# Kernel tuning notes

Measured on AMD Instinct MI355X. Metric: run time of the kernel, lower is better.

The kernel has to match this reference:

```python
import jax, jax.numpy as jnp
import numpy as np
from jax.scipy.linalg import expm

N_WIRES = 9
N_LAYERS = 4
EMBED = 512
BATCH = 64
D = 2 ** N_WIRES
P = N_WIRES * N_LAYERS * 2  # gate angles per sample


def _apply_gate(st, g, w):
    # st: (D, 2,...,2) complex64; apply 2x2 gate g on wire w
    st = jnp.moveaxis(st, 1 + w, -1)
    st = st @ g.T  # new[a] = sum_b g[a,b] old[b]
    return jnp.moveaxis(st, -1, 1 + w)


def _apply_cnot(st, c, t):
    st = jnp.moveaxis(st, (1 + c, 1 + t), (-2, -1))
    st = jnp.concatenate([st[..., 0:1, :], st[..., 1:2, ::-1]], axis=-2)
    return jnp.moveaxis(st, (-2, -1), (1 + c, 1 + t))


def _build_unitary(params):
    # simulate circuit on all D basis states at once (identity input)
    st = jnp.eye(D, dtype=jnp.complex64).reshape((D,) + (2,) * N_WIRES)
    idx = 0
    for _ in range(N_LAYERS):
        for w in range(N_WIRES):
            thy = params[idx]
            thz = params[idx + 1]
            idx += 2
            c = jnp.cos(thy * 0.5).astype(jnp.complex64)
            s = jnp.sin(thy * 0.5).astype(jnp.complex64)
            ry = jnp.stack([jnp.stack([c, -s]), jnp.stack([s, c])])
            ep = jnp.exp(0.5j * thz.astype(jnp.complex64))  # exp(i*thz/2)
            zero = jnp.zeros((), jnp.complex64)
            rz = jnp.stack([jnp.stack([jnp.conj(ep), zero]), jnp.stack([zero, ep])])
            st = _apply_gate(st, rz @ ry, w)  # Ry then Rz, fused
        for w in range(N_WIRES - 1):
            st = _apply_cnot(st, w, w + 1)
        st = _apply_cnot(st, N_WIRES - 1, 0)  # ring entangler (n_wires>1)
    # row index = input basis state i -> column i of U; take real part
    return jnp.real(st.reshape(D, D)).T


def _forward(t, w1, b1, w2, b2):
    h = jax.nn.silu(t[:, None] @ w1 + b1)          # (B, EMBED)
    params = h @ w2 + b2                            # (B, P)
    p_sg = jax.lax.stop_gradient(params)            # torch uses .detach() for the circuit
    U_stack = jax.vmap(_build_unitary)(p_sg)        # (B, D, D)
    B = t.shape[0]
    A = jnp.zeros((B, D * D), params.dtype).at[:, :P].set(params).reshape(B, D, D)
    A_skew = (A - jnp.swapaxes(A, -1, -2)) * 0.01
    U_diff = jax.vmap(expm)(A_skew)                 # (B, D, D)
    return jnp.einsum('bij,bjk->bik', U_stack, U_diff)


def setup_inputs() -> dict:
    key = jax.random.key(0)
    k_t, k1, kb1, k2, kb2 = jax.random.split(key, 5)
    t = jax.random.normal(k_t, (BATCH,), jnp.float32)
    w1 = jax.random.normal(k1, (1, EMBED), jnp.float32)
    b1 = jax.random.normal(kb1, (EMBED,), jnp.float32) * 0.1
    w2 = jax.random.normal(k2, (EMBED, P), jnp.float32) / np.sqrt(EMBED)
    b2 = jax.random.normal(kb2, (P,), jnp.float32) * 0.1
    return {"t": t, "w1": w1, "b1": b1, "w2": w2, "b2": b2}


def reference(t, w1, b1, w2, b2):
    return _forward(t, w1, b1, w2, b2)
```

## Files before the change

kernel.cpp:

```cpp
#include <hip/hip_runtime.h>
#include <math.h>


__device__ __forceinline__ float2 cmul(float2 a, float2 b){
  return make_float2(fmaf(a.x, b.x, -a.y*b.y), fmaf(a.x, b.y, a.y*b.x));
}

__device__ __forceinline__ float2 pk_fma_lo(float2 a, float2 b, float2 c){
  float2 d;
  asm("v_pk_fma_f32 %0, %1, %2, %3 op_sel:[0,0,0] op_sel_hi:[0,1,1]"
      : "=v"(d) : "v"(a), "v"(b), "v"(c));
  return d;
}
__device__ __forceinline__ float2 pk_fma_hi(float2 a, float2 b, float2 c){
  float2 d;
  asm("v_pk_fma_f32 %0, %1, %2, %3 op_sel:[1,0,0] op_sel_hi:[1,1,1]"
      : "=v"(d) : "v"(a), "v"(b), "v"(c));
  return d;
}
__device__ __forceinline__ float2 pk_mul_hi(float2 a, float2 b){
  float2 d;
  asm("v_pk_mul_f32 %0, %1, %2 op_sel:[1,0] op_sel_hi:[1,1]"
      : "=v"(d) : "v"(a), "v"(b));
  return d;
}

__device__ __forceinline__ int Fperm(int x){
  int S = x ^ (x >> 1); S ^= S >> 2; S ^= S >> 4; S ^= S >> 8;
  return (S & 0xFF) | ((((x >> 8) ^ S) & 1) << 8);
}
__device__ __forceinline__ int physmap(int x){ return x ^ ((x >> 4) & 15); }

template<int STRIDE>
__device__ __forceinline__ void apply_gate_pk(float2 amp[8], const float4* gq){
  const float4 a0 = gq[0], a1 = gq[1], a2 = gq[2], a3 = gq[3];
  const float2 P00 = make_float2(a0.x,a0.y), Q00 = make_float2(a0.z,a0.w);
  const float2 P01 = make_float2(a1.x,a1.y), Q01 = make_float2(a1.z,a1.w);
  const float2 P10 = make_float2(a2.x,a2.y), Q10 = make_float2(a2.z,a2.w);
  const float2 P11 = make_float2(a3.x,a3.y), Q11 = make_float2(a3.z,a3.w);
  #pragma unroll
  for (int b = 0; b < 8; ++b){
    if (b & STRIDE) continue;
    const float2 u = amp[b], v = amp[b + STRIDE];
    amp[b]          = pk_fma_lo(u,P00, pk_fma_hi(u,Q00, pk_fma_lo(v,P01, pk_mul_hi(v,Q01))));
    amp[b + STRIDE] = pk_fma_lo(u,P10, pk_fma_hi(u,Q10, pk_fma_lo(v,P11, pk_mul_hi(v,Q11))));
  }
}

__global__ __launch_bounds__(576)
void prep_kernel(const float* __restrict__ t,  const float* __restrict__ w1,
                 const float* __restrict__ b1, const float* __restrict__ w2,
                 const float* __restrict__ b2, float* __restrict__ prep){
  __shared__ float sh[512];
  __shared__ float part[8][72];
  __shared__ float spar[72];
  const int s = blockIdx.x;
  const float ts = t[s];
  for (int k = threadIdx.x; k < 512; k += 576){
    const float z = fmaf(ts, w1[k], b1[k]);
    sh[k] = z / (1.f + expf(-z));
  }
  __syncthreads();
  {
    const int p = threadIdx.x % 72, c = threadIdx.x / 72;
    float acc = 0.f;
    const int k0 = c*64;
    for (int k = k0; k < k0 + 64; ++k) acc = fmaf(sh[k], w2[k*72 + p], acc);
    part[c][p] = acc;
  }
  __syncthreads();
  if (threadIdx.x < 72){
    const int p = threadIdx.x;
    float acc = b2[p];
    #pragma unroll
    for (int c = 0; c < 8; ++c) acc += part[c][p];
    spar[p] = acc;
  }
  __syncthreads();
  float* pb = prep + s*768;
  if (threadIdx.x < 36){
    const int g = threadIdx.x;
    const float thy = spar[2*g], thz = spar[2*g + 1];
    float sy, cy, zi, zr;
    sincosf(0.5f*thy, &sy, &cy);
    sincosf(0.5f*thz, &zi, &zr);
    float4* gq = (float4*)(pb + g*16);
    gq[0] = make_float4( zr*cy, -zi*cy,  zi*cy,  zr*cy);
    gq[1] = make_float4(-zr*sy,  zi*sy, -zi*sy, -zr*sy);
    gq[2] = make_float4( zr*sy,  zi*sy, -zi*sy,  zr*sy);
    gq[3] = make_float4( zr*cy,  zi*cy, -zi*cy,  zr*cy);
  }
  if (threadIdx.x >= 64 && threadIdx.x < 136){
    const int j = threadIdx.x - 64;
    pb[576 + j] = (j == 0) ? 0.f : 0.01f*spar[j];
  }
  if (threadIdx.x == 0){
    float th2 = 0.f;
    for (int j = 1; j < 72; ++j){ const float v = 0.01f*spar[j]; th2 = fmaf(v, v, th2); }
    const float th = sqrtf(th2);
    float alpha, beta;
    if (th > 1e-6f){
      alpha = sinf(th)/th;
      const float s2 = sinf(0.5f*th);
      beta = 2.f*s2*s2/th2;
    } else { alpha = 1.f - th2/6.f; beta = 0.5f; }
    pb[648] = cosf(th);
    pb[649] = alpha;
    pb[650] = beta;
  }
}

__global__ __launch_bounds__(512, 6)
void sim_kernel(const float* __restrict__ prep, float* __restrict__ out){
  __shared__ __align__(16) float2 st[8][512];
  const int s    = blockIdx.x & 63;
  const int cb   = blockIdx.x >> 6;
  const int wid  = threadIdx.x >> 6;
  const int lane = threadIdx.x & 63;
  const int col  = cb*8 + wid;
  const float* gp = prep + s*768;
  float2* const S = st[wid];

  float2 amp[8];
  {
    float2 base = make_float2(1.f, 0.f);
    #pragma unroll
    for (int w = 0; w < 6; ++w){
      const int xb = (lane >> (5 - w)) & 1;
      const int ib = (col  >> (8 - w)) & 1;
      const float2 ge = *(const float2*)(gp + 16*w + (xb*2 + ib)*4);
      base = cmul(base, ge);
    }
    const int i6 = (col >> 2) & 1, i7 = (col >> 1) & 1, i8 = col & 1;
    float2 G6[2], G7[2], G8[2];
    #pragma unroll
    for (int r = 0; r < 2; ++r){
      G6[r] = *(const float2*)(gp + 16*6 + (r*2 + i6)*4);
      G7[r] = *(const float2*)(gp + 16*7 + (r*2 + i7)*4);
      G8[r] = *(const float2*)(gp + 16*8 + (r*2 + i8)*4);
    }
    #pragma unroll
    for (int j = 0; j < 8; ++j){
      const float2 tj = cmul(cmul(G6[(j>>2)&1], G7[(j>>1)&1]), G8[j&1]);
      amp[j] = cmul(base, tj);
    }
    const int bFI = physmap(Fperm(lane << 3));
    #pragma unroll
    for (int j = 0; j < 8; ++j) S[bFI ^ physmap(Fperm(j))] = amp[j];
  }

  const int base1 = (lane << 3) ^ ((lane >> 1) & 15);
  const int hq = lane >> 3, lq = lane & 7;
  const int base2 = (hq << 6) ^ ((hq << 2) & 15) ^ lq;
  const int base3 = lane ^ (lane >> 4);
  const int baseF = physmap(Fperm(lane));

  #pragma unroll
  for (int L = 1; L < 4; ++L){
    const float* gl = gp + L*9*16;
    #pragma unroll
    for (int j = 0; j < 8; ++j) amp[j] = S[base1 ^ j];
    apply_gate_pk<4>(amp, (const float4*)(gl + 6*16));
    apply_gate_pk<2>(amp, (const float4*)(gl + 7*16));
    apply_gate_pk<1>(amp, (const float4*)(gl + 8*16));
    #pragma unroll
    for (int j = 0; j < 8; ++j) S[base1 ^ j] = amp[j];
    #pragma unroll
    for (int j = 0; j < 8; ++j) amp[j] = S[base2 ^ ((j << 3) ^ (j >> 1))];
    apply_gate_pk<4>(amp, (const float4*)(gl + 3*16));
    apply_gate_pk<2>(amp, (const float4*)(gl + 4*16));
    apply_gate_pk<1>(amp, (const float4*)(gl + 5*16));
    #pragma unroll
    for (int j = 0; j < 8; ++j) S[base2 ^ ((j << 3) ^ (j >> 1))] = amp[j];
    #pragma unroll
    for (int j = 0; j < 8; ++j) amp[j] = S[base3 ^ ((j << 6) ^ ((4*j) & 15))];
    apply_gate_pk<4>(amp, (const float4*)(gl + 0*16));
    apply_gate_pk<2>(amp, (const float4*)(gl + 1*16));
    apply_gate_pk<1>(amp, (const float4*)(gl + 2*16));
    #pragma unroll
    for (int j = 0; j < 8; ++j) S[baseF ^ physmap(Fperm(j << 6))] = amp[j];
  }

  __syncthreads();
  #pragma unroll
  for (int rep = 0; rep < 2; ++rep){
    const int a  = (threadIdx.x >> 1) + rep*256;
    const int q  = threadIdx.x & 1;
    const int pa = a ^ ((a >> 4) & 15);
    float4 vv;
    vv.x = st[q*4 + 0][pa].x;
    vv.y = st[q*4 + 1][pa].x;
    vv.z = st[q*4 + 2][pa].x;
    vv.w = st[q*4 + 3][pa].x;
    *(float4*)&out[(size_t)s*262144 + (size_t)a*512 + cb*8 + q*4] = vv;
  }
}

__global__ __launch_bounds__(288)
void corr_kernel(const float* __restrict__ prep, float* __restrict__ out){
  __shared__ float part[16][18];
  __shared__ float srow[16][2];
  const int s  = blockIdx.x >> 5;
  const int rg = blockIdx.x & 31;
  const float* pp = prep + s*768;
  const int lr = threadIdx.x / 18;
  const int q  = threadIdx.x - lr*18;
  float* rowp = out + (size_t)s*262144 + (size_t)(rg*16 + lr)*512;
  const float4 x  = *(const float4*)(rowp + q*4);
  const float4 vv = *(const float4*)(pp + 576 + q*4);
  part[lr][q] = fmaf(x.x,vv.x, fmaf(x.y,vv.y, fmaf(x.z,vv.z, x.w*vv.w)));
  __syncthreads();
  if (threadIdx.x < 16){
    const int row = threadIdx.x;
    float uv = 0.f;
    #pragma unroll
    for (int k = 0; k < 18; ++k) uv += part[row][k];
    const float u0 = out[(size_t)s*262144 + (size_t)(rg*16 + row)*512];
    const float cth = pp[648], alpha = pp[649], beta = pp[650];
    srow[row][0] = fmaf(alpha, u0, -beta*uv);
    srow[row][1] = cth*u0 - alpha*uv;
  }
  __syncthreads();
  const float w = srow[lr][0];
  float4 o;
  o.x = fmaf(w, vv.x, x.x); o.y = fmaf(w, vv.y, x.y);
  o.z = fmaf(w, vv.z, x.z); o.w = fmaf(w, vv.w, x.w);
  if (q == 0) o.x = srow[lr][1];
  *(float4*)(rowp + q*4) = o;
}

extern "C" void kernel_launch(void* const* d_in, const int* in_sizes, int n_in,
                              void* d_out, int out_size, void* d_ws, size_t ws_size,
                              hipStream_t stream){
  const float* t  = (const float*)d_in[0];
  const float* w1 = (const float*)d_in[1];
  const float* b1 = (const float*)d_in[2];
  const float* w2 = (const float*)d_in[3];
  const float* b2 = (const float*)d_in[4];
  float* out  = (float*)d_out;
  float* prep = (float*)d_ws;
  prep_kernel<<<64,   576, 0, stream>>>(t, w1, b1, w2, b2, prep);
  sim_kernel <<<4096, 512, 0, stream>>>(prep, out);
  corr_kernel<<<2048, 288, 0, stream>>>(prep, out);
}
```

Measured before the change: 172.8 us.

## Split gates into real Ry rotations plus deferred diagonal Rz phase

Each fused complex Rz·Ry gate in layers 1-3 becomes a real Ry rotation, applied with scalar-operand packed FMAs (two ops per output instead of four). The Rz phases for a layer are commuted through the rotations and applied as one diagonal multiply per amplitude, built from a per-lane factor and a per-register factor that prep_kernel precomputes. The prep layout and offsets change to match, and the occupancy hint is raised from 6 to 8 waves. This trades complex FMA work for a per-layer phase multiply and extra loads of prep data.

Result: faster. 148.7 us (-13.9%).

```diff
diff --git a/kernel.cpp b/kernel.cpp
--- a/kernel.cpp
+++ b/kernel.cpp
@@ -6,22 +6,46 @@
   return make_float2(fmaf(a.x, b.x, -a.y*b.y), fmaf(a.x, b.y, a.y*b.x));
 }
 
-__device__ __forceinline__ float2 pk_fma_lo(float2 a, float2 b, float2 c){
+__device__ __forceinline__ float2 pk_fma_s_lo(float2 s2, float2 b, float2 c){
+  float2 d;
+  asm("v_pk_fma_f32 %0, %1, %2, %3 op_sel:[0,0,0] op_sel_hi:[0,1,1]"
+      : "=v"(d) : "s"(s2), "v"(b), "v"(c));
+  return d;
+}
+__device__ __forceinline__ float2 pk_mul_s_hi(float2 s2, float2 b){
+  float2 d;
+  asm("v_pk_mul_f32 %0, %1, %2 op_sel:[1,0] op_sel_hi:[1,1]"
+      : "=v"(d) : "s"(s2), "v"(b));
+  return d;
+}
+__device__ __forceinline__ float2 pk_fma_vs_lo(float2 a, float2 b, float2 c){
+  float2 d;
+  asm("v_pk_fma_f32 %0, %1, %2, %3 op_sel:[0,0,0] op_sel_hi:[0,1,1]"
+      : "=v"(d) : "v"(a), "s"(b), "v"(c));
+  return d;
+}
+__device__ __forceinline__ float2 pk_mul_vs_hi(float2 a, float2 b){
+  float2 d;
+  asm("v_pk_mul_f32 %0, %1, %2 op_sel:[1,0] op_sel_hi:[1,1]"
+      : "=v"(d) : "v"(a), "s"(b));
+  return d;
+}
+__device__ __forceinline__ float2 pk_fma_vv_lo(float2 a, float2 b, float2 c){
   float2 d;
   asm("v_pk_fma_f32 %0, %1, %2, %3 op_sel:[0,0,0] op_sel_hi:[0,1,1]"
       : "=v"(d) : "v"(a), "v"(b), "v"(c));
   return d;
 }
-__device__ __forceinline__ float2 pk_fma_hi(float2 a, float2 b, float2 c){
-  float2 d;
-  asm("v_pk_fma_f32 %0, %1, %2, %3 op_sel:[1,0,0] op_sel_hi:[1,1,1]"
-      : "=v"(d) : "v"(a), "v"(b), "v"(c));
-  return d;
-}
-__device__ __forceinline__ float2 pk_mul_hi(float2 a, float2 b){
+__device__ __forceinline__ float2 pk_mul_vv_hi(float2 a, float2 b){
   float2 d;
   asm("v_pk_mul_f32 %0, %1, %2 op_sel:[1,0] op_sel_hi:[1,1]"
       : "=v"(d) : "v"(a), "v"(b));
+  return d;
+}
+__device__ __forceinline__ float2 pk_swapneg(float2 c, float2 n){
+  float2 d;
+  asm("v_pk_mul_f32 %0, %1, %2 op_sel:[1,0] op_sel_hi:[0,1]"
+      : "=v"(d) : "v"(c), "v"(n));
   return d;
 }
 
@@ -32,18 +56,15 @@
 __device__ __forceinline__ int physmap(int x){ return x ^ ((x >> 4) & 15); }
 
 template<int STRIDE>
-__device__ __forceinline__ void apply_gate_pk(float2 amp[8], const float4* gq){
-  const float4 a0 = gq[0], a1 = gq[1], a2 = gq[2], a3 = gq[3];
-  const float2 P00 = make_float2(a0.x,a0.y), Q00 = make_float2(a0.z,a0.w);
-  const float2 P01 = make_float2(a1.x,a1.y), Q01 = make_float2(a1.z,a1.w);
-  const float2 P10 = make_float2(a2.x,a2.y), Q10 = make_float2(a2.z,a2.w);
-  const float2 P11 = make_float2(a3.x,a3.y), Q11 = make_float2(a3.z,a3.w);
+__device__ __forceinline__ void apply_rot(float2 amp[8], const float2* rp){
+  const float2 R0 = rp[0];
+  const float2 R1 = rp[1];
   #pragma unroll
   for (int b = 0; b < 8; ++b){
     if (b & STRIDE) continue;
     const float2 u = amp[b], v = amp[b + STRIDE];
-    amp[b]          = pk_fma_lo(u,P00, pk_fma_hi(u,Q00, pk_fma_lo(v,P01, pk_mul_hi(v,Q01))));
-    amp[b + STRIDE] = pk_fma_lo(u,P10, pk_fma_hi(u,Q10, pk_fma_lo(v,P11, pk_mul_hi(v,Q11))));
+    amp[b]          = pk_fma_s_lo(R0, u, pk_mul_s_hi(R0, v));
+    amp[b + STRIDE] = pk_fma_s_lo(R1, u, pk_mul_s_hi(R1, v));
   }
 }
 
@@ -77,24 +98,53 @@
     spar[p] = acc;
   }
   __syncthreads();
-  float* pb = prep + s*768;
-  if (threadIdx.x < 36){
-    const int g = threadIdx.x;
-    const float thy = spar[2*g], thz = spar[2*g + 1];
+  float* pb = prep + s*1024;
+  const int tid = threadIdx.x;
+  if (tid < 192){
+    const int l = tid >> 6, m = tid & 63;
+    float2 acc = make_float2(1.f, 0.f);
+    #pragma unroll
+    for (int w = 3; w < 9; ++w){
+      const float thz = spar[2*(9*(l+1) + w) + 1];
+      float zi, zr; sincosf(0.5f*thz, &zi, &zr);
+      const int bit = (m >> (8 - w)) & 1;
+      acc = cmul(acc, make_float2(zr, bit ? zi : -zi));
+    }
+    pb[128 + l*256 + 128 + m*2]     = acc.x;
+    pb[128 + l*256 + 128 + m*2 + 1] = acc.y;
+  } else if (tid < 216){
+    const int q = tid - 192, l = q >> 3, j = q & 7;
+    float2 acc = make_float2(1.f, 0.f);
+    #pragma unroll
+    for (int w = 0; w < 3; ++w){
+      const float thz = spar[2*(9*(l+1) + w) + 1];
+      float zi, zr; sincosf(0.5f*thz, &zi, &zr);
+      const int bit = (j >> (2 - w)) & 1;
+      acc = cmul(acc, make_float2(zr, bit ? zi : -zi));
+    }
+    float* o = pb + 128 + l*256 + 64 + j*4;
+    o[0] = acc.x; o[1] = acc.y; o[2] = -acc.y; o[3] = acc.x;
+  } else if (tid < 243){
+    const int q = tid - 216, l = q / 9, w = q - l*9;
+    const float thy = spar[2*(9*(l+1) + w)];
+    float sy, cy; sincosf(0.5f*thy, &sy, &cy);
+    float* o = pb + 128 + l*256 + w*4;
+    o[0] = cy; o[1] = -sy; o[2] = sy; o[3] = cy;
+  } else if (tid < 252){
+    const int w = tid - 243;
+    const float thy = spar[2*w], thz = spar[2*w + 1];
     float sy, cy, zi, zr;
     sincosf(0.5f*thy, &sy, &cy);
     sincosf(0.5f*thz, &zi, &zr);
-    float4* gq = (float4*)(pb + g*16);
-    gq[0] = make_float4( zr*cy, -zi*cy,  zi*cy,  zr*cy);
-    gq[1] = make_float4(-zr*sy,  zi*sy, -zi*sy, -zr*sy);
-    gq[2] = make_float4( zr*sy,  zi*sy, -zi*sy,  zr*sy);
-    gq[3] = make_float4( zr*cy,  zi*cy, -zi*cy,  zr*cy);
-  }
-  if (threadIdx.x >= 64 && threadIdx.x < 136){
-    const int j = threadIdx.x - 64;
-    pb[576 + j] = (j == 0) ? 0.f : 0.01f*spar[j];
-  }
-  if (threadIdx.x == 0){
+    float* o = pb + w*8;
+    o[0] =  zr*cy; o[1] = -zi*cy;
+    o[2] = -zr*sy; o[3] =  zi*sy;
+    o[4] =  zr*sy; o[5] =  zi*sy;
+    o[6] =  zr*cy; o[7] =  zi*cy;
+  } else if (tid < 324){
+    const int j = tid - 252;
+    pb[896 + j] = (j == 0) ? 0.f : 0.01f*spar[j];
+  } else if (tid == 324){
     float th2 = 0.f;
     for (int j = 1; j < 72; ++j){ const float v = 0.01f*spar[j]; th2 = fmaf(v, v, th2); }
     const float th = sqrtf(th2);
@@ -104,13 +154,13 @@
       const float s2 = sinf(0.5f*th);
       beta = 2.f*s2*s2/th2;
     } else { alpha = 1.f - th2/6.f; beta = 0.5f; }
-    pb[648] = cosf(th);
-    pb[649] = alpha;
-    pb[650] = beta;
-  }
-}
-
-__global__ __launch_bounds__(512, 6)
+    pb[968] = cosf(th);
+    pb[969] = alpha;
+    pb[970] = beta;
+  }
+}
+
+__global__ __launch_bounds__(512, 8)
 void sim_kernel(const float* __restrict__ prep, float* __restrict__ out){
   __shared__ __align__(16) float2 st[8][512];
   const int s    = blockIdx.x & 63;
@@ -118,8 +168,9 @@
   const int wid  = threadIdx.x >> 6;
   const int lane = threadIdx.x & 63;
   const int col  = cb*8 + wid;
-  const float* gp = prep + s*768;
+  const float* gp = prep + s*1024;
   float2* const S = st[wid];
+  const float2 NEG1P1 = make_float2(-1.f, 1.f);
 
   float2 amp[8];
   {
@@ -128,16 +179,16 @@
     for (int w = 0; w < 6; ++w){
       const int xb = (lane >> (5 - w)) & 1;
       const int ib = (col  >> (8 - w)) & 1;
-      const float2 ge = *(const float2*)(gp + 16*w + (xb*2 + ib)*4);
+      const float2 ge = *(const float2*)(gp + 8*w + (xb*2 + ib)*2);
       base = cmul(base, ge);
     }
     const int i6 = (col >> 2) & 1, i7 = (col >> 1) & 1, i8 = col & 1;
     float2 G6[2], G7[2], G8[2];
     #pragma unroll
     for (int r = 0; r < 2; ++r){
-      G6[r] = *(const float2*)(gp + 16*6 + (r*2 + i6)*4);
-      G7[r] = *(const float2*)(gp + 16*7 + (r*2 + i7)*4);
-      G8[r] = *(const float2*)(gp + 16*8 + (r*2 + i8)*4);
+      G6[r] = *(const float2*)(gp + 8*6 + (r*2 + i6)*2);
+      G7[r] = *(const float2*)(gp + 8*7 + (r*2 + i7)*2);
+      G8[r] = *(const float2*)(gp + 8*8 + (r*2 + i8)*2);
     }
     #pragma unroll
     for (int j = 0; j < 8; ++j){
@@ -156,27 +207,38 @@
   const int baseF = physmap(Fperm(lane));
 
   #pragma unroll
-  for (int L = 1; L < 4; ++L){
-    const float* gl = gp + L*9*16;
+  for (int L = 0; L < 3; ++L){
+    const float* lb = gp + 128 + L*256;
     #pragma unroll
     for (int j = 0; j < 8; ++j) amp[j] = S[base1 ^ j];
-    apply_gate_pk<4>(amp, (const float4*)(gl + 6*16));
-    apply_gate_pk<2>(amp, (const float4*)(gl + 7*16));
-    apply_gate_pk<1>(amp, (const float4*)(gl + 8*16));
+    apply_rot<4>(amp, (const float2*)(lb + 6*4));
+    apply_rot<2>(amp, (const float2*)(lb + 7*4));
+    apply_rot<1>(amp, (const float2*)(lb + 8*4));
     #pragma unroll
     for (int j = 0; j < 8; ++j) S[base1 ^ j] = amp[j];
     #pragma unroll
     for (int j = 0; j < 8; ++j) amp[j] = S[base2 ^ ((j << 3) ^ (j >> 1))];
-    apply_gate_pk<4>(amp, (const float4*)(gl + 3*16));
-    apply_gate_pk<2>(amp, (const float4*)(gl + 4*16));
-    apply_gate_pk<1>(amp, (const float4*)(gl + 5*16));
+    apply_rot<4>(amp, (const float2*)(lb + 3*4));
+    apply_rot<2>(amp, (const float2*)(lb + 4*4));
+    apply_rot<1>(amp, (const float2*)(lb + 5*4));
     #pragma unroll
     for (int j = 0; j < 8; ++j) S[base2 ^ ((j << 3) ^ (j >> 1))] = amp[j];
     #pragma unroll
     for (int j = 0; j < 8; ++j) amp[j] = S[base3 ^ ((j << 6) ^ ((4*j) & 15))];
-    apply_gate_pk<4>(amp, (const float4*)(gl + 0*16));
-    apply_gate_pk<2>(amp, (const float4*)(gl + 1*16));
-    apply_gate_pk<1>(amp, (const float4*)(gl + 2*16));
+    apply_rot<4>(amp, (const float2*)(lb + 0*4));
+    apply_rot<2>(amp, (const float2*)(lb + 1*4));
+    apply_rot<1>(amp, (const float2*)(lb + 2*4));
+    {
+      const float2 A = *(const float2*)(lb + 128 + lane*2);
+      #pragma unroll
+      for (int j = 0; j < 8; ++j){
+        const float2 P = *(const float2*)(lb + 64 + j*4);
+        const float2 Q = *(const float2*)(lb + 64 + j*4 + 2);
+        const float2 C = pk_fma_vs_lo(A, P, pk_mul_vs_hi(A, Q));
+        const float2 Dn = pk_swapneg(C, NEG1P1);
+        amp[j] = pk_fma_vv_lo(amp[j], C, pk_mul_vv_hi(amp[j], Dn));
+      }
+    }
     #pragma unroll
     for (int j = 0; j < 8; ++j) S[baseF ^ physmap(Fperm(j << 6))] = amp[j];
   }
@@ -202,12 +264,12 @@
   __shared__ float srow[16][2];
   const int s  = blockIdx.x >> 5;
   const int rg = blockIdx.x & 31;
-  const float* pp = prep + s*768;
+  const float* pp = prep + s*1024;
   const int lr = threadIdx.x / 18;
   const int q  = threadIdx.x - lr*18;
   float* rowp = out + (size_t)s*262144 + (size_t)(rg*16 + lr)*512;
   const float4 x  = *(const float4*)(rowp + q*4);
-  const float4 vv = *(const float4*)(pp + 576 + q*4);
+  const float4 vv = *(const float4*)(pp + 896 + q*4);
   part[lr][q] = fmaf(x.x,vv.x, fmaf(x.y,vv.y, fmaf(x.z,vv.z, x.w*vv.w)));
   __syncthreads();
   if (threadIdx.x < 16){
@@ -216,7 +278,7 @@
     #pragma unroll
     for (int k = 0; k < 18; ++k) uv += part[row][k];
     const float u0 = out[(size_t)s*262144 + (size_t)(rg*16 + row)*512];
-    const float cth = pp[648], alpha = pp[649], beta = pp[650];
+    const float cth = pp[968], alpha = pp[969], beta = pp[970];
     srow[row][0] = fmaf(alpha, u0, -beta*uv);
     srow[row][1] = cth*u0 - alpha*uv;
   }
```

## Fuse parameter prep into sim kernel and factor Rz gates into diagonal phases

Applied to the files above, without the earlier changes.

Drops the separate prep kernel. Each sim block now recomputes the MLP, sin/cos and gate tables into LDS, which removes one launch and the global round-trip. Layers 2-4 split each gate into a real Ry rotation followed by one combined diagonal phase built from precomputed per-index angle tables, so the per-gate complex multiplies shrink. The corr kernel is restructured into fewer, larger blocks that reduce with wavefront shuffles instead of LDS. In exchange, every one of the 4096 blocks redoes a 512x72 matvec, which adds redundant compute and w2 reads.

Result: slower. 187.9 us (+8.8%).

```diff
diff --git a/kernel.cpp b/kernel.cpp
--- a/kernel.cpp
+++ b/kernel.cpp
@@ -5,25 +5,24 @@
 __device__ __forceinline__ float2 cmul(float2 a, float2 b){
   return make_float2(fmaf(a.x, b.x, -a.y*b.y), fmaf(a.x, b.y, a.y*b.x));
 }
-
 __device__ __forceinline__ float2 pk_fma_lo(float2 a, float2 b, float2 c){
   float2 d;
   asm("v_pk_fma_f32 %0, %1, %2, %3 op_sel:[0,0,0] op_sel_hi:[0,1,1]"
       : "=v"(d) : "v"(a), "v"(b), "v"(c));
   return d;
 }
-__device__ __forceinline__ float2 pk_fma_hi(float2 a, float2 b, float2 c){
-  float2 d;
-  asm("v_pk_fma_f32 %0, %1, %2, %3 op_sel:[1,0,0] op_sel_hi:[1,1,1]"
-      : "=v"(d) : "v"(a), "v"(b), "v"(c));
-  return d;
-}
 __device__ __forceinline__ float2 pk_mul_hi(float2 a, float2 b){
   float2 d;
   asm("v_pk_mul_f32 %0, %1, %2 op_sel:[1,0] op_sel_hi:[1,1]"
       : "=v"(d) : "v"(a), "v"(b));
   return d;
 }
+__device__ __forceinline__ float2 pk_swapneg(float2 c, float2 n){
+  float2 d;
+  asm("v_pk_mul_f32 %0, %1, %2 op_sel:[1,0] op_sel_hi:[0,1]"
+      : "=v"(d) : "v"(c), "v"(n));
+  return d;
+}
 
 __device__ __forceinline__ int Fperm(int x){
   int S = x ^ (x >> 1); S ^= S >> 2; S ^= S >> 4; S ^= S >> 8;
@@ -32,69 +31,104 @@
 __device__ __forceinline__ int physmap(int x){ return x ^ ((x >> 4) & 15); }
 
 template<int STRIDE>
-__device__ __forceinline__ void apply_gate_pk(float2 amp[8], const float4* gq){
-  const float4 a0 = gq[0], a1 = gq[1], a2 = gq[2], a3 = gq[3];
-  const float2 P00 = make_float2(a0.x,a0.y), Q00 = make_float2(a0.z,a0.w);
-  const float2 P01 = make_float2(a1.x,a1.y), Q01 = make_float2(a1.z,a1.w);
-  const float2 P10 = make_float2(a2.x,a2.y), Q10 = make_float2(a2.z,a2.w);
-  const float2 P11 = make_float2(a3.x,a3.y), Q11 = make_float2(a3.z,a3.w);
+__device__ __forceinline__ void apply_rot(float2 amp[8], float4 rc){
+  const float2 R0 = make_float2(rc.x, rc.y);
+  const float2 R1 = make_float2(rc.z, rc.w);
   #pragma unroll
   for (int b = 0; b < 8; ++b){
     if (b & STRIDE) continue;
     const float2 u = amp[b], v = amp[b + STRIDE];
-    amp[b]          = pk_fma_lo(u,P00, pk_fma_hi(u,Q00, pk_fma_lo(v,P01, pk_mul_hi(v,Q01))));
-    amp[b + STRIDE] = pk_fma_lo(u,P10, pk_fma_hi(u,Q10, pk_fma_lo(v,P11, pk_mul_hi(v,Q11))));
-  }
-}
-
-__global__ __launch_bounds__(576)
-void prep_kernel(const float* __restrict__ t,  const float* __restrict__ w1,
-                 const float* __restrict__ b1, const float* __restrict__ w2,
-                 const float* __restrict__ b2, float* __restrict__ prep){
-  __shared__ float sh[512];
-  __shared__ float part[8][72];
+    amp[b]          = pk_fma_lo(R0, u, pk_mul_hi(R0, v));
+    amp[b + STRIDE] = pk_fma_lo(R1, u, pk_mul_hi(R1, v));
+  }
+}
+
+#define LDS_L1G 0
+#define LDS_ROT 72
+#define LDS_BPH 180
+#define LDS_APH 288
+#define BUF_FLOATS 1160
+
+__global__ __launch_bounds__(512, 6)
+void sim_kernel(const float* __restrict__ t,  const float* __restrict__ w1,
+                const float* __restrict__ b1, const float* __restrict__ w2,
+                const float* __restrict__ b2,
+                float* __restrict__ out, float* __restrict__ ws){
+  __shared__ __align__(16) float2 st[8][512];
+  __shared__ __align__(16) float buf[BUF_FLOATS];
   __shared__ float spar[72];
-  const int s = blockIdx.x;
-  const float ts = t[s];
-  for (int k = threadIdx.x; k < 512; k += 576){
-    const float z = fmaf(ts, w1[k], b1[k]);
-    sh[k] = z / (1.f + expf(-z));
-  }
-  __syncthreads();
+  const int s    = blockIdx.x & 63;
+  const int cb   = blockIdx.x >> 6;
+  const int tid  = threadIdx.x;
+  const int wid  = tid >> 6;
+  const int lane = tid & 63;
+  const int col  = cb*8 + wid;
+  float2* const S = st[wid];
+  const float2 NEG1P1 = make_float2(-1.f, 1.f);
+
   {
-    const int p = threadIdx.x % 72, c = threadIdx.x / 72;
-    float acc = 0.f;
-    const int k0 = c*64;
-    for (int k = k0; k < k0 + 64; ++k) acc = fmaf(sh[k], w2[k*72 + p], acc);
-    part[c][p] = acc;
-  }
-  __syncthreads();
-  if (threadIdx.x < 72){
-    const int p = threadIdx.x;
-    float acc = b2[p];
-    #pragma unroll
-    for (int c = 0; c < 8; ++c) acc += part[c][p];
-    spar[p] = acc;
-  }
-  __syncthreads();
-  float* pb = prep + s*768;
-  if (threadIdx.x < 36){
-    const int g = threadIdx.x;
-    const float thy = spar[2*g], thz = spar[2*g + 1];
+    const float ts = t[s];
+    const float z = fmaf(ts, w1[tid], b1[tid]);
+    buf[tid] = z / (1.f + expf(-z));
+  }
+  __syncthreads();
+  {
+    const int c = tid >> 7, p = tid & 127;
+    if (p < 72){
+      float acc = 0.f;
+      const int k0 = c*128;
+      #pragma unroll 4
+      for (int k = k0; k < k0+128; ++k) acc = fmaf(buf[k], w2[k*72 + p], acc);
+      buf[512 + c*72 + p] = acc;
+    }
+  }
+  __syncthreads();
+  if (tid < 72)
+    spar[tid] = b2[tid] + buf[512+tid] + buf[584+tid] + buf[656+tid] + buf[728+tid];
+  __syncthreads();
+  if (tid < 27){
+    const int l = tid/9, w = tid - l*9;
+    const float thy = spar[2*(9*(l+1) + w)];
+    float sy, cy; sincosf(0.5f*thy, &sy, &cy);
+    float* o = buf + LDS_ROT + tid*4;
+    o[0] = cy; o[1] = -sy; o[2] = sy; o[3] = cy;
+  } else if (tid >= 32 && tid < 41){
+    const int w = tid - 32;
+    const float thy = spar[2*w], thz = spar[2*w + 1];
     float sy, cy, zi, zr;
     sincosf(0.5f*thy, &sy, &cy);
     sincosf(0.5f*thz, &zi, &zr);
-    float4* gq = (float4*)(pb + g*16);
-    gq[0] = make_float4( zr*cy, -zi*cy,  zi*cy,  zr*cy);
-    gq[1] = make_float4(-zr*sy,  zi*sy, -zi*sy, -zr*sy);
-    gq[2] = make_float4( zr*sy,  zi*sy, -zi*sy,  zr*sy);
-    gq[3] = make_float4( zr*cy,  zi*cy, -zi*cy,  zr*cy);
-  }
-  if (threadIdx.x >= 64 && threadIdx.x < 136){
-    const int j = threadIdx.x - 64;
-    pb[576 + j] = (j == 0) ? 0.f : 0.01f*spar[j];
-  }
-  if (threadIdx.x == 0){
+    float* o = buf + LDS_L1G + w*8;
+    o[0] =  zr*cy; o[1] = -zi*cy;
+    o[2] = -zr*sy; o[3] =  zi*sy;
+    o[4] =  zr*sy; o[5] =  zi*sy;
+    o[6] =  zr*cy; o[7] =  zi*cy;
+  } else if (tid >= 64 && tid < 88){
+    const int q = tid - 64, l = q >> 3, j = q & 7;
+    float ang = 0.f;
+    #pragma unroll
+    for (int w = 0; w < 3; ++w){
+      const float thz = spar[2*(9*(l+1) + w) + 1];
+      ang += ((j >> (2 - w)) & 1) ? thz : -thz;
+    }
+    float si, co; sincosf(0.5f*ang, &si, &co);
+    float* o = buf + LDS_BPH + q*4;
+    o[0] = co; o[1] = si; o[2] = -si; o[3] = co;
+  } else if (tid >= 128 && tid < 320){
+    const int q = tid - 128, l = q >> 6, m = q & 63;
+    float ang = 0.f;
+    #pragma unroll
+    for (int w = 3; w < 9; ++w){
+      const float thz = spar[2*(9*(l+1) + w) + 1];
+      ang += ((m >> (8 - w)) & 1) ? thz : -thz;
+    }
+    float si, co; sincosf(0.5f*ang, &si, &co);
+    float* o = buf + LDS_APH + q*2;
+    o[0] = co; o[1] = si;
+  } else if (cb == 0 && tid >= 320 && tid < 392){
+    const int j = tid - 320;
+    ws[s*80 + j] = (j == 0) ? 0.f : 0.01f*spar[j];
+  } else if (cb == 0 && tid == 392){
     float th2 = 0.f;
     for (int j = 1; j < 72; ++j){ const float v = 0.01f*spar[j]; th2 = fmaf(v, v, th2); }
     const float th = sqrtf(th2);
@@ -104,22 +138,11 @@
       const float s2 = sinf(0.5f*th);
       beta = 2.f*s2*s2/th2;
     } else { alpha = 1.f - th2/6.f; beta = 0.5f; }
-    pb[648] = cosf(th);
-    pb[649] = alpha;
-    pb[650] = beta;
-  }
-}
-
-__global__ __launch_bounds__(512, 6)
-void sim_kernel(const float* __restrict__ prep, float* __restrict__ out){
-  __shared__ __align__(16) float2 st[8][512];
-  const int s    = blockIdx.x & 63;
-  const int cb   = blockIdx.x >> 6;
-  const int wid  = threadIdx.x >> 6;
-  const int lane = threadIdx.x & 63;
-  const int col  = cb*8 + wid;
-  const float* gp = prep + s*768;
-  float2* const S = st[wid];
+    ws[s*80 + 72] = cosf(th);
+    ws[s*80 + 73] = alpha;
+    ws[s*80 + 74] = beta;
+  }
+  __syncthreads();
 
   float2 amp[8];
   {
@@ -128,16 +151,16 @@
     for (int w = 0; w < 6; ++w){
       const int xb = (lane >> (5 - w)) & 1;
       const int ib = (col  >> (8 - w)) & 1;
-      const float2 ge = *(const float2*)(gp + 16*w + (xb*2 + ib)*4);
+      const float2 ge = *(const float2*)&buf[LDS_L1G + 8*w + (xb*2 + ib)*2];
       base = cmul(base, ge);
     }
     const int i6 = (col >> 2) & 1, i7 = (col >> 1) & 1, i8 = col & 1;
     float2 G6[2], G7[2], G8[2];
     #pragma unroll
     for (int r = 0; r < 2; ++r){
-      G6[r] = *(const float2*)(gp + 16*6 + (r*2 + i6)*4);
-      G7[r] = *(const float2*)(gp + 16*7 + (r*2 + i7)*4);
-      G8[r] = *(const float2*)(gp + 16*8 + (r*2 + i8)*4);
+      G6[r] = *(const float2*)&buf[LDS_L1G + 48 + (r*2 + i6)*2];
+      G7[r] = *(const float2*)&buf[LDS_L1G + 56 + (r*2 + i7)*2];
+      G8[r] = *(const float2*)&buf[LDS_L1G + 64 + (r*2 + i8)*2];
     }
     #pragma unroll
     for (int j = 0; j < 8; ++j){
@@ -156,27 +179,38 @@
   const int baseF = physmap(Fperm(lane));
 
   #pragma unroll
-  for (int L = 1; L < 4; ++L){
-    const float* gl = gp + L*9*16;
+  for (int L = 0; L < 3; ++L){
     #pragma unroll
     for (int j = 0; j < 8; ++j) amp[j] = S[base1 ^ j];
-    apply_gate_pk<4>(amp, (const float4*)(gl + 6*16));
-    apply_gate_pk<2>(amp, (const float4*)(gl + 7*16));
-    apply_gate_pk<1>(amp, (const float4*)(gl + 8*16));
+    apply_rot<4>(amp, *(const float4*)&buf[LDS_ROT + (L*9 + 6)*4]);
+    apply_rot<2>(amp, *(const float4*)&buf[LDS_ROT + (L*9 + 7)*4]);
+    apply_rot<1>(amp, *(const float4*)&buf[LDS_ROT + (L*9 + 8)*4]);
     #pragma unroll
     for (int j = 0; j < 8; ++j) S[base1 ^ j] = amp[j];
     #pragma unroll
     for (int j = 0; j < 8; ++j) amp[j] = S[base2 ^ ((j << 3) ^ (j >> 1))];
-    apply_gate_pk<4>(amp, (const float4*)(gl + 3*16));
-    apply_gate_pk<2>(amp, (const float4*)(gl + 4*16));
-    apply_gate_pk<1>(amp, (const float4*)(gl + 5*16));
+    apply_rot<4>(amp, *(const float4*)&buf[LDS_ROT + (L*9 + 3)*4]);
+    apply_rot<2>(amp, *(const float4*)&buf[LDS_ROT + (L*9 + 4)*4]);
+    apply_rot<1>(amp, *(const float4*)&buf[LDS_ROT + (L*9 + 5)*4]);
     #pragma unroll
     for (int j = 0; j < 8; ++j) S[base2 ^ ((j << 3) ^ (j >> 1))] = amp[j];
     #pragma unroll
     for (int j = 0; j < 8; ++j) amp[j] = S[base3 ^ ((j << 6) ^ ((4*j) & 15))];
-    apply_gate_pk<4>(amp, (const float4*)(gl + 0*16));
-    apply_gate_pk<2>(amp, (const float4*)(gl + 1*16));
-    apply_gate_pk<1>(amp, (const float4*)(gl + 2*16));
+    apply_rot<4>(amp, *(const float4*)&buf[LDS_ROT + (L*9 + 0)*4]);
+    apply_rot<2>(amp, *(const float4*)&buf[LDS_ROT + (L*9 + 1)*4]);
+    apply_rot<1>(amp, *(const float4*)&buf[LDS_ROT + (L*9 + 2)*4]);
+    {
+      const float2 A = *(const float2*)&buf[LDS_APH + (L*64 + lane)*2];
+      #pragma unroll
+      for (int j = 0; j < 8; ++j){
+        const float4 bq = *(const float4*)&buf[LDS_BPH + (L*8 + j)*4];
+        const float2 P = make_float2(bq.x, bq.y);
+        const float2 Q = make_float2(bq.z, bq.w);
+        const float2 C  = pk_fma_lo(A, P, pk_mul_hi(A, Q));
+        const float2 Dn = pk_swapneg(C, NEG1P1);
+        amp[j] = pk_fma_lo(amp[j], C, pk_mul_hi(amp[j], Dn));
+      }
+    }
     #pragma unroll
     for (int j = 0; j < 8; ++j) S[baseF ^ physmap(Fperm(j << 6))] = amp[j];
   }
@@ -184,8 +218,8 @@
   __syncthreads();
   #pragma unroll
   for (int rep = 0; rep < 2; ++rep){
-    const int a  = (threadIdx.x >> 1) + rep*256;
-    const int q  = threadIdx.x & 1;
+    const int a  = (tid >> 1) + rep*256;
+    const int q  = tid & 1;
     const int pa = a ^ ((a >> 4) & 15);
     float4 vv;
     vv.x = st[q*4 + 0][pa].x;
@@ -196,37 +230,38 @@
   }
 }
 
-__global__ __launch_bounds__(288)
-void corr_kernel(const float* __restrict__ prep, float* __restrict__ out){
-  __shared__ float part[16][18];
-  __shared__ float srow[16][2];
-  const int s  = blockIdx.x >> 5;
-  const int rg = blockIdx.x & 31;
-  const float* pp = prep + s*768;
-  const int lr = threadIdx.x / 18;
-  const int q  = threadIdx.x - lr*18;
-  float* rowp = out + (size_t)s*262144 + (size_t)(rg*16 + lr)*512;
-  const float4 x  = *(const float4*)(rowp + q*4);
-  const float4 vv = *(const float4*)(pp + 576 + q*4);
-  part[lr][q] = fmaf(x.x,vv.x, fmaf(x.y,vv.y, fmaf(x.z,vv.z, x.w*vv.w)));
-  __syncthreads();
-  if (threadIdx.x < 16){
-    const int row = threadIdx.x;
-    float uv = 0.f;
-    #pragma unroll
-    for (int k = 0; k < 18; ++k) uv += part[row][k];
-    const float u0 = out[(size_t)s*262144 + (size_t)(rg*16 + row)*512];
-    const float cth = pp[648], alpha = pp[649], beta = pp[650];
-    srow[row][0] = fmaf(alpha, u0, -beta*uv);
-    srow[row][1] = cth*u0 - alpha*uv;
-  }
-  __syncthreads();
-  const float w = srow[lr][0];
-  float4 o;
-  o.x = fmaf(w, vv.x, x.x); o.y = fmaf(w, vv.y, x.y);
-  o.z = fmaf(w, vv.z, x.z); o.w = fmaf(w, vv.w, x.w);
-  if (q == 0) o.x = srow[lr][1];
-  *(float4*)(rowp + q*4) = o;
+__global__ __launch_bounds__(256)
+void corr_kernel(const float* __restrict__ ws, float* __restrict__ out){
+  const int s   = blockIdx.x >> 3;
+  const int rg  = blockIdx.x & 7;
+  const int qi  = threadIdx.x & 3;
+  const int row = rg*64 + (threadIdx.x >> 2);
+  const float* vp = ws + s*80;
+  float* rowp = out + (size_t)s*262144 + (size_t)row*512;
+  float2 x[9], vv[9];
+  #pragma unroll
+  for (int i = 0; i < 9; ++i){
+    x[i]  = *(const float2*)(rowp + (qi*9 + i)*2);
+    vv[i] = *(const float2*)(vp   + (qi*9 + i)*2);
+  }
+  float uv = 0.f;
+  #pragma unroll
+  for (int i = 0; i < 9; ++i)
+    uv = fmaf(x[i].x, vv[i].x, fmaf(x[i].y, vv[i].y, uv));
+  uv += __shfl_xor(uv, 1);
+  uv += __shfl_xor(uv, 2);
+  const float u0  = __shfl(x[0].x, 0, 4);
+  const float cth = vp[72], alpha = vp[73], beta = vp[74];
+  const float w  = fmaf(alpha, u0, -beta*uv);
+  const float c0 = cth*u0 - alpha*uv;
+  #pragma unroll
+  for (int i = 0; i < 9; ++i){
+    float2 o;
+    o.x = fmaf(w, vv[i].x, x[i].x);
+    o.y = fmaf(w, vv[i].y, x[i].y);
+    if (qi == 0 && i == 0) o.x = c0;
+    *(float2*)(rowp + (qi*9 + i)*2) = o;
+  }
 }
 
 extern "C" void kernel_launch(void* const* d_in, const int* in_sizes, int n_in,
@@ -237,9 +272,8 @@
   const float* b1 = (const float*)d_in[2];
   const float* w2 = (const float*)d_in[3];
   const float* b2 = (const float*)d_in[4];
-  float* out  = (float*)d_out;
-  float* prep = (float*)d_ws;
-  prep_kernel<<<64,   576, 0, stream>>>(t, w1, b1, w2, b2, prep);
-  sim_kernel <<<4096, 512, 0, stream>>>(prep, out);
-  corr_kernel<<<2048, 288, 0, stream>>>(prep, out);
-}
+  float* out = (float*)d_out;
+  float* ws  = (float*)d_ws;
+  sim_kernel <<<4096, 512, 0, stream>>>(t, w1, b1, w2, b2, out, ws);
+  corr_kernel<<<512,  256, 0, stream>>>(ws, out);
+}
```
